# Performance work log

Measured on AMD Instinct MI355X. Metric: run time of the kernel, lower is better.

## Reference

```python
import jax, jax.numpy as jnp
import numpy as np

EPS = 1e-8

def setup_inputs() -> dict:
    key = jax.random.key(0)
    k1, k2, k3 = jax.random.split(key, 3)
    B, N, C = 4, 2048, 512
    x = jax.random.normal(k1, (B, N, C), dtype=jnp.float32)
    w_qkv = jax.random.normal(k2, (C, 3 * C), dtype=jnp.float32) * (C ** -0.5)
    w_proj = jax.random.normal(k3, (C, C), dtype=jnp.float32) * (C ** -0.5)
    b_proj = jnp.zeros((C,), dtype=jnp.float32)
    alpha = jnp.ones((1,), dtype=jnp.float32)
    beta = jnp.ones((1,), dtype=jnp.float32)
    return {"x": x, "w_qkv": w_qkv, "alpha": alpha, "beta": beta,
            "w_proj": w_proj, "b_proj": b_proj}

def reference(x, w_qkv, alpha, beta, w_proj, b_proj):
    B, N, C = x.shape
    H = 8  # num_heads
    D = C // H  # head_dim = 64
    scale = D ** -0.5
    qkv = (x @ w_qkv).reshape(B, N, 3, H, D)
    q = jnp.transpose(qkv[:, :, 0], (0, 2, 1, 3))  # (B,H,N,D)
    k = jnp.transpose(qkv[:, :, 1], (0, 2, 1, 3))
    v = jnp.transpose(qkv[:, :, 2], (0, 2, 1, 3))
    attn = jnp.einsum('bhnd,bhmd->bhnm', q, k) * scale  # (B,H,N,N)
    # sparse branch: relu^2 sum-normalize
    sp = jnp.square(jax.nn.relu(attn))
    attn_sparse = sp / (sp.sum(axis=-1, keepdims=True) + EPS)
    # dense branch: softmax
    attn_dense = jax.nn.softmax(attn, axis=-1)
    a = jax.nn.sigmoid(alpha)
    b = jax.nn.sigmoid(beta)
    wsum = a + b + EPS
    attn_final = (a / wsum) * attn_sparse + (b / wsum) * attn_dense
    out = jnp.einsum('bhnm,bhmd->bhnd', attn_final, v)  # (B,H,N,D)
    out = jnp.transpose(out, (0, 2, 1, 3)).reshape(B, N, C)
    return out @ w_proj + b_proj
```

## Files before the change

### kernel.cpp

```cpp
#include <hip/hip_runtime.h>

typedef unsigned short u16;
typedef unsigned int   u32;
typedef __attribute__((ext_vector_type(8))) __bf16 bf16x8;
typedef __attribute__((ext_vector_type(4))) float  f32x4;
typedef __attribute__((ext_vector_type(4))) u32    u32x4;

#define AS1q __attribute__((address_space(1)))
#define AS3q __attribute__((address_space(3)))

static __device__ __forceinline__ u16 f2bf(float f) {
    u32 u = __builtin_bit_cast(u32, f);
    u32 r = u + 0x7FFFu + ((u >> 16) & 1u);
    return (u16)(r >> 16);
}

static __device__ __forceinline__ bf16x8 ld16(const u16* p) {
    return __builtin_bit_cast(bf16x8, *(const float4*)(const void*)p);
}

static __device__ __forceinline__ f32x4 mfma16(bf16x8 a, bf16x8 b, f32x4 c) {
    return __builtin_amdgcn_mfma_f32_16x16x32_bf16(a, b, c, 0, 0, 0);
}

static __device__ __forceinline__ void gld16(const u16* g, u16* l) {
    __builtin_amdgcn_global_load_lds((const AS1q u32*)g, (AS3q u32*)l, 16, 0, 0);
}

static __device__ __forceinline__ float exp2_fast(float v) {
    float e;
    asm("v_exp_f32 %0, %1" : "=v"(e) : "v"(v));
    return e;
}

static __device__ __forceinline__ u32 cvtpk(float lo, float hi_) {
    u32 d;
    asm("v_cvt_pk_bf16_f32 %0, %1, %2" : "=v"(d) : "v"(lo), "v"(hi_));
    return d;
}

__global__ __launch_bounds__(256) void k_cast_x(const float* __restrict__ x, u16* __restrict__ xb) {
    int i = blockIdx.x * 256 + threadIdx.x;
    float4 v = ((const float4*)x)[i];
    ushort4 o;
    o.x = f2bf(v.x); o.y = f2bf(v.y); o.z = f2bf(v.z); o.w = f2bf(v.w);
    ((ushort4*)xb)[i] = o;
}

__global__ __launch_bounds__(256) void k_transpose_cast(const float* __restrict__ in, u16* __restrict__ out,
                                                        int K, int Nn) {
    __shared__ float tile[32][33];
    int tx = threadIdx.x & 31, ty = threadIdx.x >> 5;
    int k0 = blockIdx.y * 32, n0 = blockIdx.x * 32;
#pragma unroll
    for (int i = 0; i < 4; ++i)
        tile[ty + i * 8][tx] = in[(k0 + ty + i * 8) * Nn + n0 + tx];
    __syncthreads();
#pragma unroll
    for (int i = 0; i < 4; ++i)
        out[(n0 + ty + i * 8) * K + k0 + tx] = f2bf(tile[tx][ty + i * 8]);
}

static __device__ __forceinline__ void stage128x64(const u16* __restrict__ gbase, int ld,
                                                   u16* lds, int tid) {
    int wid = tid >> 6;
#pragma unroll
    for (int i = 0; i < 4; ++i) {
        int idx = i * 256 + tid;
        int row = idx >> 3, c8 = idx & 7;
        int csw = c8 ^ (row & 7);
        gld16(gbase + row * ld + csw * 8, lds + (i * 256 + wid * 64) * 8);
    }
}

static __device__ __forceinline__ bf16x8 frag(const u16* lds, int row, int col16) {
    return ld16(lds + row * 64 + ((col16 ^ (row & 7)) << 3));
}

__global__ __launch_bounds__(256) void k_gemm_qkv(const u16* __restrict__ xb, const u16* __restrict__ wT,
                                                  u16* __restrict__ Qh, u16* __restrict__ Kh,
                                                  u16* __restrict__ VTh) {
    __shared__ __align__(16) u16 at[128 * 64];
    __shared__ __align__(16) u16 bt[128 * 64];
    int tid = threadIdx.x, lane = tid & 63, wid = tid >> 6;
    int tm = blockIdx.x / 12, tn = blockIdx.x % 12;
    int rb = tm * 128, cb = tn * 128;
    int wr = (wid >> 1) * 64, wc = (wid & 1) * 64;
    int l15 = lane & 15, lhi = lane >> 4;
    f32x4 acc[4][4] = {};
    for (int kk = 0; kk < 512; kk += 64) {
        stage128x64(xb + rb * 512 + kk, 512, at, tid);
        stage128x64(wT + cb * 512 + kk, 512, bt, tid);
        __syncthreads();
        bf16x8 af[4][2], bfr[4][2];
#pragma unroll
        for (int m = 0; m < 4; ++m) {
            int row = wr + m * 16 + l15;
            af[m][0] = frag(at, row, lhi);
            af[m][1] = frag(at, row, 4 + lhi);
        }
#pragma unroll
        for (int n = 0; n < 4; ++n) {
            int row = wc + n * 16 + l15;
            bfr[n][0] = frag(bt, row, lhi);
            bfr[n][1] = frag(bt, row, 4 + lhi);
        }
#pragma unroll
        for (int m = 0; m < 4; ++m)
#pragma unroll
            for (int n = 0; n < 4; ++n) {
                acc[m][n] = mfma16(af[m][0], bfr[n][0], acc[m][n]);
                acc[m][n] = mfma16(af[m][1], bfr[n][1], acc[m][n]);
            }
        __syncthreads();
    }
#pragma unroll
    for (int m = 0; m < 4; ++m)
#pragma unroll
        for (int n = 0; n < 4; ++n)
#pragma unroll
            for (int r = 0; r < 4; ++r) {
                int R  = rb + wr + m * 16 + lhi * 4 + r;
                int Cg = cb + wc + n * 16 + l15;
                int b = R >> 11, nseq = R & 2047;
                int s = Cg >> 9, rm = Cg & 511, h = rm >> 6, d = rm & 63;
                int bh = (b << 3) + h;
                float v = acc[m][n][r];
                if (s == 0)      Qh[(bh * 2048 + nseq) * 64 + d] = f2bf(v * 0.1803368801111244f);
                else if (s == 1) Kh[(bh * 2048 + nseq) * 64 + d] = f2bf(v);
                else             VTh[(bh * 64 + d) * 2048 + nseq] = f2bf(v);
            }
}

__global__ __launch_bounds__(256) void k_attn(const u16* __restrict__ Qh, const u16* __restrict__ Kh,
                                              const u16* __restrict__ VTh, const float* __restrict__ alpha,
                                              const float* __restrict__ beta, u16* __restrict__ AO) {
    __shared__ __align__(16) u16 kls[2][32 * 64];
    __shared__ __align__(16) u16 vls[2][64 * 32];
    int tid = threadIdx.x, lane = tid & 63, wid = tid >> 6;
    int l15 = lane & 15, lhi = lane >> 4;
    int wg = (blockIdx.x & 7) * 128 + (blockIdx.x >> 3);
    int bh = wg >> 5;
    int qb = (wg & 31) << 6;
    const u16* Qp = Qh + bh * (2048 * 64);
    const u16* Kp = Kh + bh * (2048 * 64);
    const u16* Vp = VTh + bh * (2048 * 64);
    int qbase = qb + wid * 16;
    bf16x8 qa0 = ld16(Qp + (qbase + l15) * 64 + lhi * 8);
    bf16x8 qa1 = ld16(Qp + (qbase + l15) * 64 + 32 + lhi * 8);
    int kap = 8 * (l15 >> 2) + 4 * ((l15 >> 1) & 1) + (l15 & 1);
    f32x4 accd[4] = {}, accs[4] = {};
    float dend = 0.f, dens = 0.f;
    const f32x4 z = {0.f, 0.f, 0.f, 0.f};

    int krow = tid >> 3, kc8 = tid & 7;
    int vrow = tid >> 2, vc4 = tid & 3;
    const u16* kg = Kp + krow * 64 + ((kc8 ^ (krow & 7)) << 3);
    const u16* vg = Vp + vrow * 2048 + ((vc4 ^ (vrow & 3)) << 3);

    gld16(kg, &kls[0][0] + tid * 8);
    gld16(vg, &vls[0][0] + tid * 8);
    asm volatile("s_waitcnt vmcnt(0)" ::: "memory");
    __builtin_amdgcn_s_barrier();

    for (int kb = 0; kb < 2048; kb += 32) {
        int cur = (kb >> 5) & 1;
        if (kb + 32 < 2048) {
            gld16(kg + (kb + 32) * 64, &kls[cur ^ 1][0] + tid * 8);
            gld16(vg + (kb + 32), &vls[cur ^ 1][0] + tid * 8);
            asm volatile("s_waitcnt vmcnt(2)" ::: "memory");
        } else {
            asm volatile("s_waitcnt vmcnt(0)" ::: "memory");
        }
        __builtin_amdgcn_s_barrier();
        f32x4 s[2];
#pragma unroll
        for (int kt = 0; kt < 2; ++kt) {
            int row = kap + 2 * kt;
            bf16x8 kf0 = ld16(&kls[cur][0] + row * 64 + ((lhi ^ (row & 7)) << 3));
            bf16x8 kf1 = ld16(&kls[cur][0] + row * 64 + (((4 + lhi) ^ (row & 7)) << 3));
            s[kt] = mfma16(kf0, qa0, z);
            s[kt] = mfma16(kf1, qa1, s[kt]);
        }
        float ed[2][4], ps[2][4];
#pragma unroll
        for (int kt = 0; kt < 2; ++kt)
#pragma unroll
            for (int r = 0; r < 4; ++r) {
                float v = s[kt][r];
                float e = exp2_fast(v);
                float t = fmaxf(v, 0.f);
                float p = t * t;
                dend += e;
                dens += p;
                ed[kt][r] = e;
                ps[kt][r] = p;
            }
        bf16x8 pfd = __builtin_bit_cast(bf16x8, (u32x4){
            cvtpk(ed[0][0], ed[0][1]), cvtpk(ed[1][0], ed[1][1]),
            cvtpk(ed[0][2], ed[0][3]), cvtpk(ed[1][2], ed[1][3])});
        bf16x8 pfs = __builtin_bit_cast(bf16x8, (u32x4){
            cvtpk(ps[0][0], ps[0][1]), cvtpk(ps[1][0], ps[1][1]),
            cvtpk(ps[0][2], ps[0][3]), cvtpk(ps[1][2], ps[1][3])});
#pragma unroll
        for (int n = 0; n < 4; ++n) {
            int row = n * 16 + l15;
            bf16x8 vf = ld16(&vls[cur][0] + row * 32 + ((lhi ^ (row & 3)) << 3));
            accd[n] = mfma16(pfd, vf, accd[n]);
            accs[n] = mfma16(pfs, vf, accs[n]);
        }
        asm volatile("" ::: "memory");
        __builtin_amdgcn_s_barrier();
    }
    dend += __shfl_xor(dend, 16); dend += __shfl_xor(dend, 32);
    dens += __shfl_xor(dens, 16); dens += __shfl_xor(dens, 32);
    float sa = 1.f / (1.f + __expf(-alpha[0]));
    float sb = 1.f / (1.f + __expf(-beta[0]));
    float wsum = sa + sb + 1e-8f;
    float wa = sa / wsum, wb = sb / wsum;
    int b = bh >> 3, h = bh & 7;
    float id[4], isr[4];
#pragma unroll
    for (int r = 0; r < 4; ++r) {
        float dd = __shfl(dend, lhi * 4 + r);
        float ds = __shfl(dens, lhi * 4 + r);
        id[r] = wb / dd;
        isr[r] = wa / (ds + 1e-8f);
    }
#pragma unroll
    for (int n = 0; n < 4; ++n)
#pragma unroll
        for (int r = 0; r < 4; ++r) {
            int R  = b * 2048 + qbase + lhi * 4 + r;
            int Cg = h * 64 + n * 16 + l15;
            float o = isr[r] * accs[n][r] + id[r] * accd[n][r];
            AO[R * 512 + Cg] = f2bf(o);
        }
}

__global__ __launch_bounds__(256) void k_gemm_proj(const u16* __restrict__ AO, const u16* __restrict__ wT,
                                                   const float* __restrict__ bproj, float* __restrict__ out) {
    __shared__ __align__(16) u16 at[128 * 64];
    __shared__ __align__(16) u16 bt[128 * 64];
    int tid = threadIdx.x, lane = tid & 63, wid = tid >> 6;
    int tm = blockIdx.x >> 2, tn = blockIdx.x & 3;
    int rb = tm * 128, cb = tn * 128;
    int wr = (wid >> 1) * 64, wc = (wid & 1) * 64;
    int l15 = lane & 15, lhi = lane >> 4;
    f32x4 acc[4][4] = {};
    for (int kk = 0; kk < 512; kk += 64) {
        stage128x64(AO + rb * 512 + kk, 512, at, tid);
        stage128x64(wT + cb * 512 + kk, 512, bt, tid);
        __syncthreads();
        bf16x8 af[4][2], bfr[4][2];
#pragma unroll
        for (int m = 0; m < 4; ++m) {
            int row = wr + m * 16 + l15;
            af[m][0] = frag(at, row, lhi);
            af[m][1] = frag(at, row, 4 + lhi);
        }
#pragma unroll
        for (int n = 0; n < 4; ++n) {
            int row = wc + n * 16 + l15;
            bfr[n][0] = frag(bt, row, lhi);
            bfr[n][1] = frag(bt, row, 4 + lhi);
        }
#pragma unroll
        for (int m = 0; m < 4; ++m)
#pragma unroll
            for (int n = 0; n < 4; ++n) {
                acc[m][n] = mfma16(af[m][0], bfr[n][0], acc[m][n]);
                acc[m][n] = mfma16(af[m][1], bfr[n][1], acc[m][n]);
            }
        __syncthreads();
    }
#pragma unroll
    for (int m = 0; m < 4; ++m)
#pragma unroll
        for (int n = 0; n < 4; ++n)
#pragma unroll
            for (int r = 0; r < 4; ++r) {
                int R  = rb + wr + m * 16 + lhi * 4 + r;
                int Cg = cb + wc + n * 16 + l15;
                out[R * 512 + Cg] = acc[m][n][r] + bproj[Cg];
            }
}

extern "C" void kernel_launch(void* const* d_in, const int* in_sizes, int n_in,
                              void* d_out, int out_size, void* d_ws, size_t ws_size,
                              hipStream_t stream) {
    const float* x      = (const float*)d_in[0];
    const float* w_qkv  = (const float*)d_in[1];
    const float* alpha  = (const float*)d_in[2];
    const float* beta   = (const float*)d_in[3];
    const float* w_proj = (const float*)d_in[4];
    const float* b_proj = (const float*)d_in[5];
    float* out = (float*)d_out;
    char* w = (char*)d_ws;
    u16* xb     = (u16*)(w);
    u16* wqkvT  = (u16*)(w + 8388608);
    u16* wprojT = (u16*)(w + 9961472);
    u16* Qh     = (u16*)(w + 10485760);
    u16* Kh     = (u16*)(w + 18874368);
    u16* VTh    = (u16*)(w + 27262976);
    u16* AO     = xb;

    k_cast_x<<<dim3(4096), dim3(256), 0, stream>>>(x, xb);
    k_transpose_cast<<<dim3(48, 16), dim3(256), 0, stream>>>(w_qkv, wqkvT, 512, 1536);
    k_transpose_cast<<<dim3(16, 16), dim3(256), 0, stream>>>(w_proj, wprojT, 512, 512);
    k_gemm_qkv<<<dim3(768), dim3(256), 0, stream>>>(xb, wqkvT, Qh, Kh, VTh);
    k_attn<<<dim3(1024), dim3(256), 0, stream>>>(Qh, Kh, VTh, alpha, beta, AO);
    k_gemm_proj<<<dim3(256), dim3(256), 0, stream>>>(AO, wprojT, b_proj, out);
}
```

Before: 147.6 us.

## Process two 16-row query groups per wave to reuse K/V tiles

Each wave now handles 32 query rows instead of 16, so every K and V fragment loaded from LDS feeds two sets of MFMAs. The workgroup covers 128 queries and the grid is halved to 512 blocks. The KV loop is manually unrolled by two with fixed ping-pong buffers, which removes the per-iteration buffer index computation. In exchange, accumulator registers double, which may lower occupancy, and fewer blocks are available to fill the CUs.

```diff
diff --git a/kernel.cpp b/kernel.cpp
--- a/kernel.cpp
+++ b/kernel.cpp
@@ -132,6 +132,55 @@
             }
 }
 
+#define ATTN_STEP(BUF)                                                           \
+    {                                                                            \
+        f32x4 s[2][2];                                                           \
+        _Pragma("unroll")                                                        \
+        for (int kt = 0; kt < 2; ++kt) {                                         \
+            int row = kap + 2 * kt;                                              \
+            const u16* kbp = &kls[BUF][0] + row * 64;                            \
+            bf16x8 kf0 = ld16(kbp + ((lhi ^ (row & 7)) << 3));                   \
+            bf16x8 kf1 = ld16(kbp + (((4 + lhi) ^ (row & 7)) << 3));             \
+            _Pragma("unroll")                                                    \
+            for (int qg = 0; qg < 2; ++qg) {                                     \
+                s[qg][kt] = mfma16(kf0, qa[qg][0], z);                           \
+                s[qg][kt] = mfma16(kf1, qa[qg][1], s[qg][kt]);                   \
+            }                                                                    \
+        }                                                                        \
+        bf16x8 pfd[2], pfs[2];                                                   \
+        _Pragma("unroll")                                                        \
+        for (int qg = 0; qg < 2; ++qg) {                                         \
+            float ed[2][4], ps[2][4];                                            \
+            _Pragma("unroll")                                                    \
+            for (int kt = 0; kt < 2; ++kt)                                       \
+                _Pragma("unroll")                                                \
+                for (int r = 0; r < 4; ++r) {                                    \
+                    float v = s[qg][kt][r];                                      \
+                    float e = exp2_fast(v);                                      \
+                    float t = fmaxf(v, 0.f);                                     \
+                    float p = t * t;                                             \
+                    dend[qg] += e; dens[qg] += p;                                \
+                    ed[kt][r] = e; ps[kt][r] = p;                                \
+                }                                                                \
+            pfd[qg] = __builtin_bit_cast(bf16x8, (u32x4){                        \
+                cvtpk(ed[0][0], ed[0][1]), cvtpk(ed[1][0], ed[1][1]),            \
+                cvtpk(ed[0][2], ed[0][3]), cvtpk(ed[1][2], ed[1][3])});          \
+            pfs[qg] = __builtin_bit_cast(bf16x8, (u32x4){                        \
+                cvtpk(ps[0][0], ps[0][1]), cvtpk(ps[1][0], ps[1][1]),            \
+                cvtpk(ps[0][2], ps[0][3]), cvtpk(ps[1][2], ps[1][3])});          \
+        }                                                                        \
+        _Pragma("unroll")                                                        \
+        for (int n = 0; n < 4; ++n) {                                            \
+            int row = n * 16 + l15;                                              \
+            bf16x8 vf = ld16(&vls[BUF][0] + row * 32 + ((lhi ^ (row & 3)) << 3));\
+            _Pragma("unroll")                                                    \
+            for (int qg = 0; qg < 2; ++qg) {                                     \
+                accd[qg][n] = mfma16(pfd[qg], vf, accd[qg][n]);                  \
+                accs[qg][n] = mfma16(pfs[qg], vf, accs[qg][n]);                  \
+            }                                                                    \
+        }                                                                        \
+    }
+
 __global__ __launch_bounds__(256) void k_attn(const u16* __restrict__ Qh, const u16* __restrict__ Kh,
                                               const u16* __restrict__ VTh, const float* __restrict__ alpha,
                                               const float* __restrict__ beta, u16* __restrict__ AO) {
@@ -139,18 +188,23 @@
     __shared__ __align__(16) u16 vls[2][64 * 32];
     int tid = threadIdx.x, lane = tid & 63, wid = tid >> 6;
     int l15 = lane & 15, lhi = lane >> 4;
-    int wg = (blockIdx.x & 7) * 128 + (blockIdx.x >> 3);
-    int bh = wg >> 5;
-    int qb = (wg & 31) << 6;
+    int wg = (blockIdx.x & 7) * 64 + (blockIdx.x >> 3);
+    int bh = wg >> 4;
+    int qb = (wg & 15) << 7;
     const u16* Qp = Qh + bh * (2048 * 64);
     const u16* Kp = Kh + bh * (2048 * 64);
     const u16* Vp = VTh + bh * (2048 * 64);
-    int qbase = qb + wid * 16;
-    bf16x8 qa0 = ld16(Qp + (qbase + l15) * 64 + lhi * 8);
-    bf16x8 qa1 = ld16(Qp + (qbase + l15) * 64 + 32 + lhi * 8);
+    int qbase = qb + wid * 32;
+    bf16x8 qa[2][2];
+#pragma unroll
+    for (int qg = 0; qg < 2; ++qg) {
+        int row = qbase + qg * 16 + l15;
+        qa[qg][0] = ld16(Qp + row * 64 + lhi * 8);
+        qa[qg][1] = ld16(Qp + row * 64 + 32 + lhi * 8);
+    }
     int kap = 8 * (l15 >> 2) + 4 * ((l15 >> 1) & 1) + (l15 & 1);
-    f32x4 accd[4] = {}, accs[4] = {};
-    float dend = 0.f, dens = 0.f;
+    f32x4 accd[2][4] = {}, accs[2][4] = {};
+    float dend[2] = {}, dens[2] = {};
     const f32x4 z = {0.f, 0.f, 0.f, 0.f};
 
     int krow = tid >> 3, kc8 = tid & 7;
@@ -162,80 +216,61 @@
     gld16(vg, &vls[0][0] + tid * 8);
     asm volatile("s_waitcnt vmcnt(0)" ::: "memory");
     __builtin_amdgcn_s_barrier();
-
-    for (int kb = 0; kb < 2048; kb += 32) {
-        int cur = (kb >> 5) & 1;
-        if (kb + 32 < 2048) {
-            gld16(kg + (kb + 32) * 64, &kls[cur ^ 1][0] + tid * 8);
-            gld16(vg + (kb + 32), &vls[cur ^ 1][0] + tid * 8);
+    const u16* kgp = kg + 32 * 64;
+    const u16* vgp = vg + 32;
+
+    for (int kb = 0; kb < 2048; kb += 64) {
+        gld16(kgp, &kls[1][0] + tid * 8);
+        gld16(vgp, &vls[1][0] + tid * 8);
+        kgp += 32 * 64; vgp += 32;
+        asm volatile("s_waitcnt vmcnt(2)" ::: "memory");
+        __builtin_amdgcn_s_barrier();
+        ATTN_STEP(0)
+        asm volatile("" ::: "memory");
+        __builtin_amdgcn_s_barrier();
+        if (kb + 64 < 2048) {
+            gld16(kgp, &kls[0][0] + tid * 8);
+            gld16(vgp, &vls[0][0] + tid * 8);
+            kgp += 32 * 64; vgp += 32;
             asm volatile("s_waitcnt vmcnt(2)" ::: "memory");
         } else {
             asm volatile("s_waitcnt vmcnt(0)" ::: "memory");
         }
         __builtin_amdgcn_s_barrier();
-        f32x4 s[2];
-#pragma unroll
-        for (int kt = 0; kt < 2; ++kt) {
-            int row = kap + 2 * kt;
-            bf16x8 kf0 = ld16(&kls[cur][0] + row * 64 + ((lhi ^ (row & 7)) << 3));
-            bf16x8 kf1 = ld16(&kls[cur][0] + row * 64 + (((4 + lhi) ^ (row & 7)) << 3));
-            s[kt] = mfma16(kf0, qa0, z);
-            s[kt] = mfma16(kf1, qa1, s[kt]);
-        }
-        float ed[2][4], ps[2][4];
-#pragma unroll
-        for (int kt = 0; kt < 2; ++kt)
-#pragma unroll
-            for (int r = 0; r < 4; ++r) {
-                float v = s[kt][r];
-                float e = exp2_fast(v);
-                float t = fmaxf(v, 0.f);
-                float p = t * t;
-                dend += e;
-                dens += p;
-                ed[kt][r] = e;
-                ps[kt][r] = p;
-            }
-        bf16x8 pfd = __builtin_bit_cast(bf16x8, (u32x4){
-            cvtpk(ed[0][0], ed[0][1]), cvtpk(ed[1][0], ed[1][1]),
-            cvtpk(ed[0][2], ed[0][3]), cvtpk(ed[1][2], ed[1][3])});
-        bf16x8 pfs = __builtin_bit_cast(bf16x8, (u32x4){
-            cvtpk(ps[0][0], ps[0][1]), cvtpk(ps[1][0], ps[1][1]),
-            cvtpk(ps[0][2], ps[0][3]), cvtpk(ps[1][2], ps[1][3])});
-#pragma unroll
-        for (int n = 0; n < 4; ++n) {
-            int row = n * 16 + l15;
-            bf16x8 vf = ld16(&vls[cur][0] + row * 32 + ((lhi ^ (row & 3)) << 3));
-            accd[n] = mfma16(pfd, vf, accd[n]);
-            accs[n] = mfma16(pfs, vf, accs[n]);
-        }
+        ATTN_STEP(1)
         asm volatile("" ::: "memory");
         __builtin_amdgcn_s_barrier();
     }
-    dend += __shfl_xor(dend, 16); dend += __shfl_xor(dend, 32);
-    dens += __shfl_xor(dens, 16); dens += __shfl_xor(dens, 32);
+#pragma unroll
+    for (int qg = 0; qg < 2; ++qg) {
+        dend[qg] += __shfl_xor(dend[qg], 16); dend[qg] += __shfl_xor(dend[qg], 32);
+        dens[qg] += __shfl_xor(dens[qg], 16); dens[qg] += __shfl_xor(dens[qg], 32);
+    }
     float sa = 1.f / (1.f + __expf(-alpha[0]));
     float sb = 1.f / (1.f + __expf(-beta[0]));
     float wsum = sa + sb + 1e-8f;
     float wa = sa / wsum, wb = sb / wsum;
     int b = bh >> 3, h = bh & 7;
-    float id[4], isr[4];
-#pragma unroll
-    for (int r = 0; r < 4; ++r) {
-        float dd = __shfl(dend, lhi * 4 + r);
-        float ds = __shfl(dens, lhi * 4 + r);
-        id[r] = wb / dd;
-        isr[r] = wa / (ds + 1e-8f);
-    }
-#pragma unroll
-    for (int n = 0; n < 4; ++n)
+#pragma unroll
+    for (int qg = 0; qg < 2; ++qg) {
+        float id[4], isr[4];
 #pragma unroll
         for (int r = 0; r < 4; ++r) {
-            int R  = b * 2048 + qbase + lhi * 4 + r;
-            int Cg = h * 64 + n * 16 + l15;
-            float o = isr[r] * accs[n][r] + id[r] * accd[n][r];
-            AO[R * 512 + Cg] = f2bf(o);
-        }
+            float dd = __shfl(dend[qg], lhi * 4 + r);
+            float ds = __shfl(dens[qg], lhi * 4 + r);
+            id[r] = wb / dd;
+            isr[r] = wa / (ds + 1e-8f);
+        }
+#pragma unroll
+        for (int n = 0; n < 4; ++n)
+#pragma unroll
+            for (int r = 0; r < 4; ++r) {
+                int R  = b * 2048 + qbase + qg * 16 + lhi * 4 + r;
+                int Cg = h * 64 + n * 16 + l15;
+                float o = isr[r] * accs[qg][n][r] + id[r] * accd[qg][n][r];
+                AO[R * 512 + Cg] = f2bf(o);
+            }
+    }
 }
 
 __global__ __launch_bounds__(256) void k_gemm_proj(const u16* __restrict__ AO, const u16* __restrict__ wT,
@@ -309,6 +344,6 @@
     k_transpose_cast<<<dim3(48, 16), dim3(256), 0, stream>>>(w_qkv, wqkvT, 512, 1536);
     k_transpose_cast<<<dim3(16, 16), dim3(256), 0, stream>>>(w_proj, wprojT, 512, 512);
     k_gemm_qkv<<<dim3(768), dim3(256), 0, stream>>>(xb, wqkvT, Qh, Kh, VTh);
-    k_attn<<<dim3(1024), dim3(256), 0, stream>>>(Qh, Kh, VTh, alpha, beta, AO);
+    k_attn<<<dim3(512), dim3(256), 0, stream>>>(Qh, Kh, VTh, alpha, beta, AO);
     k_gemm_proj<<<dim3(256), dim3(256), 0, stream>>>(AO, wprojT, b_proj, out);
 }
```

Result: faster. 143.4 us (-2.9%).
